# Kernel optimization log

Hardware: AMD Instinct MI355X
Metric: run time of the kernel (lower is better)

The kernel has to match this reference:

```python
import jax, jax.numpy as jnp
import numpy as np

NEG = -1e9  # effectively -inf for masked logits, grad-safe

def apply_rope(t, cos, sin):
    # t: [b, H, S, D]; cos/sin: [S, D] -> rotate-half RoPE
    d = t.shape[-1]
    t1, t2 = t[..., : d // 2], t[..., d // 2 :]
    rot = jnp.concatenate([-t2, t1], axis=-1)
    return t * cos[None, None] + rot * sin[None, None]


def setup_inputs() -> dict:
    key = jax.random.key(0)
    ks = jax.random.split(key, 8)
    b, S, d_in = 1, 4096, 2048
    H, G, D = 16, 4, 128
    d_out = H * D
    sc = 1.0 / np.sqrt(d_in)
    x = jax.random.normal(ks[0], (b, S, d_in), dtype=jnp.float32)
    # causal mask: True = masked (future positions)
    mask = jnp.triu(jnp.ones((S, S), dtype=bool), k=1)
    inv = 1.0 / (10000.0 ** (jnp.arange(0, D, 2, dtype=jnp.float32) / D))
    ang = jnp.arange(S, dtype=jnp.float32)[:, None] * inv[None, :]  # [S, D/2]
    ang = jnp.concatenate([ang, ang], axis=-1)                      # [S, D]
    cos, sin = jnp.cos(ang), jnp.sin(ang)
    Wq = jax.random.normal(ks[1], (d_out, d_in), dtype=jnp.float32) * sc
    Wk = jax.random.normal(ks[2], (G * D, d_in), dtype=jnp.float32) * sc
    Wv = jax.random.normal(ks[3], (G * D, d_in), dtype=jnp.float32) * sc
    Wo = jax.random.normal(ks[4], (d_in, d_out), dtype=jnp.float32) * sc
    return {"x": x, "mask": mask, "cos": cos, "sin": sin,
            "Wq": Wq, "Wk": Wk, "Wv": Wv, "Wo": Wo}


def reference(x, mask, cos, sin, Wq, Wk, Wv, Wo):
    b, S, d_in = x.shape
    G = Wk.shape[0] // cos.shape[-1]          # num_kv_groups
    D = cos.shape[-1]                          # head_dim
    H = Wq.shape[0] // D                       # num_heads
    n = H // G                                 # group_size
    q = (x @ Wq.T).reshape(b, S, H, D).transpose(0, 2, 1, 3)   # [b,H,S,D]
    k = (x @ Wk.T).reshape(b, S, G, D).transpose(0, 2, 1, 3)   # [b,G,S,D]
    v = (x @ Wv.T).reshape(b, S, G, D).transpose(0, 2, 1, 3)
    q = apply_rope(q, cos, sin)
    k = apply_rope(k, cos, sin)
    # GQA: group heads instead of repeat_interleave (head h -> group h // n)
    qg = q.reshape(b, G, n, S, D)
    scores = jnp.einsum('bgnqd,bgkd->bgnqk', qg, k)            # [b,G,n,S,S]
    scores = jnp.where(mask[None, None, None], NEG, scores)
    w = jax.nn.softmax(scores / np.sqrt(D), axis=-1)
    ctx = jnp.einsum('bgnqk,bgkd->bgnqd', w, v)                # [b,G,n,S,D]
    ctx = ctx.reshape(b, H, S, D).transpose(0, 2, 1, 3).reshape(b, S, H * D)
    return ctx @ Wo.T
```

## Files before the change

### kernel.cpp

```cpp
#include <hip/hip_runtime.h>

typedef __attribute__((ext_vector_type(8))) short bf16x8;
typedef __attribute__((ext_vector_type(4))) short bf16x4;
typedef __attribute__((ext_vector_type(8))) unsigned short u16x8;
typedef __attribute__((ext_vector_type(4))) float f32x4;

__device__ __forceinline__ unsigned short f2b(float f) {
  unsigned int u = __builtin_bit_cast(unsigned int, f);
  u += 0x7FFFu + ((u >> 16) & 1u);
  return (unsigned short)(u >> 16);
}
__device__ __forceinline__ float b2f(unsigned short h) {
  return __builtin_bit_cast(float, ((unsigned int)h) << 16);
}

__device__ __forceinline__ f32x4 mfma16x16x16(bf16x4 a, bf16x4 b, f32x4 c) {
#if __has_builtin(__builtin_amdgcn_mfma_f32_16x16x16bf16_1k)
  return __builtin_amdgcn_mfma_f32_16x16x16bf16_1k(a, b, c, 0, 0, 0);
#else
  asm volatile("v_mfma_f32_16x16x16_bf16 %0, %1, %2, %0" : "+v"(c) : "v"(a), "v"(b));
  return c;
#endif
}

#define AS1(p) (const __attribute__((address_space(1))) void*)(p)
#define AS3(p) (__attribute__((address_space(3))) void*)(p)

__device__ __forceinline__ void cvt8(const float* __restrict__ in,
                                     unsigned short* __restrict__ out,
                                     int i, float scale) {
  const float4* p = (const float4*)in + (size_t)i * 2;
  float4 a = p[0], b = p[1];
  u16x8 r;
  r[0] = f2b(a.x * scale); r[1] = f2b(a.y * scale);
  r[2] = f2b(a.z * scale); r[3] = f2b(a.w * scale);
  r[4] = f2b(b.x * scale); r[5] = f2b(b.y * scale);
  r[6] = f2b(b.z * scale); r[7] = f2b(b.w * scale);
  *((u16x8*)out + i) = r;
}

__global__ __launch_bounds__(256) void k_cvt_all(
    const float* __restrict__ x,  const float* __restrict__ Wq,
    const float* __restrict__ Wk, const float* __restrict__ Wv,
    const float* __restrict__ Wo, unsigned short* __restrict__ xb,
    unsigned short* __restrict__ wqkv, unsigned short* __restrict__ Wob,
    float sc) {
  int bid = blockIdx.x;
  int tid = threadIdx.x;
  if (bid < 4096)      cvt8(x,  xb,             (bid        ) * 256 + tid, 1.f);
  else if (bid < 6144) cvt8(Wq, wqkv,           (bid - 4096) * 256 + tid, sc);
  else if (bid < 6656) cvt8(Wk, wqkv + 4194304, (bid - 6144) * 256 + tid, 1.f);
  else if (bid < 7168) cvt8(Wv, wqkv + 5242880, (bid - 6656) * 256 + tid, 1.f);
  else                 cvt8(Wo, Wob,            (bid - 7168) * 256 + tid, 1.f);
}

__global__ __launch_bounds__(256) void k_post(unsigned short* __restrict__ qkv,
                                              const float* __restrict__ cosb,
                                              const float* __restrict__ sinb,
                                              unsigned short* __restrict__ vT) {
  __shared__ unsigned short tile[64][72];
  const int bid = blockIdx.x, t = threadIdx.x;
  if (bid < 2560) {
    int tid = bid * 256 + t;
    int oct = tid & 7;
    int hd  = (tid >> 3) % 20;
    int s   = (tid >> 3) / 20;
    unsigned short* p1 = qkv + (size_t)s * 3072 + hd * 128 + oct * 8;
    unsigned short* p2 = p1 + 64;
    u16x8 a = *(const u16x8*)p1;
    u16x8 b = *(const u16x8*)p2;
    const float4* cp = (const float4*)(cosb + (size_t)s * 128 + oct * 8);
    const float4* sp = (const float4*)(sinb + (size_t)s * 128 + oct * 8);
    float4 c0 = cp[0], c1 = cp[1], s0 = sp[0], s1 = sp[1];
    float cs[8] = {c0.x,c0.y,c0.z,c0.w,c1.x,c1.y,c1.z,c1.w};
    float sn[8] = {s0.x,s0.y,s0.z,s0.w,s1.x,s1.y,s1.z,s1.w};
    u16x8 ra, rb;
#pragma unroll
    for (int j = 0; j < 8; ++j) {
      float av = b2f(a[j]), bv = b2f(b[j]);
      ra[j] = f2b(av * cs[j] - bv * sn[j]);
      rb[j] = f2b(bv * cs[j] + av * sn[j]);
    }
    *(u16x8*)p1 = ra;
    *(u16x8*)p2 = rb;
  } else {
    int idx = bid - 2560;
    int bs = idx >> 3, bc = idx & 7;
#pragma unroll
    for (int i = 0; i < 2; ++i) {
      int c8 = t + 256 * i;
      int row = c8 >> 3, cb = c8 & 7;
      u16x8 v = *(const u16x8*)(qkv + (size_t)(bs * 64 + row) * 3072 + 2560 + bc * 64 + cb * 8);
#pragma unroll
      for (int j = 0; j < 8; ++j) tile[row][cb * 8 + j] = v[j];
    }
    __syncthreads();
#pragma unroll
    for (int i = 0; i < 2; ++i) {
      int c8 = t + 256 * i;
      int crow = c8 >> 3, sb = c8 & 7;
      u16x8 v;
#pragma unroll
      for (int j = 0; j < 8; ++j) v[j] = tile[sb * 8 + j][crow];
      *(u16x8*)(vT + (size_t)(bc * 64 + crow) * 4096 + bs * 64 + sb * 8) = v;
    }
  }
}

template <int OUTF32>
__global__ __launch_bounds__(256) void k_gemm_bt(
    const unsigned short* __restrict__ A, const unsigned short* __restrict__ B,
    void* __restrict__ C, int K, int lda, int ldb, int ldc) {
  __shared__ unsigned short As[128 * 64];
  __shared__ unsigned short Bs[128 * 64];
  const int t = threadIdx.x;
  const int lane = t & 63, w = t >> 6;
  const int wm = w >> 1, wn = w & 1;
  const int o = blockIdx.x + blockIdx.y * gridDim.x;
  const int xcd = o & 7, j = o >> 3;
  const int per = gridDim.x >> 3;
  const int bn = xcd * per + (j % per);
  const int bm = j / per;
  const unsigned short* Arow = A + (size_t)(bm * 128) * lda;
  const unsigned short* Brow = B + (size_t)(bn * 128) * ldb;

  f32x4 acc[4][4] = {};
  for (int kt = 0; kt < K; kt += 64) {
#pragma unroll
    for (int i = 0; i < 4; ++i) {
      int idx = i * 256 + t;
      int r = idx >> 3, blk = idx & 7;
      int sb = blk ^ (r & 7);
      __builtin_amdgcn_global_load_lds(AS1(Arow + (size_t)r * lda + kt + sb * 8),
                                       AS3(As + (i * 256 + w * 64) * 8), 16, 0, 0);
    }
#pragma unroll
    for (int i = 0; i < 4; ++i) {
      int idx = i * 256 + t;
      int r = idx >> 3, blk = idx & 7;
      int sb = blk ^ (r & 7);
      __builtin_amdgcn_global_load_lds(AS1(Brow + (size_t)r * ldb + kt + sb * 8),
                                       AS3(Bs + (i * 256 + w * 64) * 8), 16, 0, 0);
    }
    __syncthreads();
#pragma unroll
    for (int kk = 0; kk < 2; ++kk) {
      bf16x8 av[4], bv[4];
#pragma unroll
      for (int i = 0; i < 4; ++i) {
        int r = wm * 64 + i * 16 + (lane & 15);
        int off = (r * 128 + (kk * 32 + (lane >> 4) * 8) * 2) ^ ((r & 7) << 4);
        av[i] = *(const bf16x8*)((const char*)As + off);
      }
#pragma unroll
      for (int j2 = 0; j2 < 4; ++j2) {
        int r = wn * 64 + j2 * 16 + (lane & 15);
        int off = (r * 128 + (kk * 32 + (lane >> 4) * 8) * 2) ^ ((r & 7) << 4);
        bv[j2] = *(const bf16x8*)((const char*)Bs + off);
      }
#pragma unroll
      for (int i = 0; i < 4; ++i)
#pragma unroll
        for (int j2 = 0; j2 < 4; ++j2)
          acc[i][j2] = __builtin_amdgcn_mfma_f32_16x16x32_bf16(av[i], bv[j2], acc[i][j2], 0, 0, 0);
    }
    __syncthreads();
  }
#pragma unroll
  for (int i = 0; i < 4; ++i)
#pragma unroll
    for (int j2 = 0; j2 < 4; ++j2)
#pragma unroll
      for (int r = 0; r < 4; ++r) {
        int m = bm * 128 + wm * 64 + i * 16 + (lane >> 4) * 4 + r;
        int n = bn * 128 + wn * 64 + j2 * 16 + (lane & 15);
        float v = acc[i][j2][r];
        if (OUTF32) ((float*)C)[(size_t)m * ldc + n] = v;
        else        ((unsigned short*)C)[(size_t)m * ldc + n] = f2b(v);
      }
}

__device__ __forceinline__ void stage_k(const unsigned short* __restrict__ qk,
                                        unsigned short* __restrict__ dst,
                                        int kt, int g, int t, int w) {
#pragma unroll
  for (int i = 0; i < 4; ++i) {
    int idx = i * 256 + t;
    int r = idx >> 4, blk = idx & 15;
    int sb = (blk & 8) | ((blk ^ r) & 7);
    __builtin_amdgcn_global_load_lds(
        AS1(qk + (size_t)(kt * 64 + r) * 3072 + 2048 + g * 128 + sb * 8),
        AS3(dst + (i * 256 + w * 64) * 8), 16, 0, 0);
  }
}
__device__ __forceinline__ void stage_v(const unsigned short* __restrict__ vT,
                                        unsigned short* __restrict__ dst,
                                        int kt, int g, int t, int w) {
#pragma unroll
  for (int i = 0; i < 4; ++i) {
    int idx = i * 256 + t;
    int r = idx >> 3, blk = idx & 7;
    int sb = blk ^ (r & 7);
    __builtin_amdgcn_global_load_lds(
        AS1(vT + (size_t)(g * 128 + r) * 4096 + kt * 64 + sb * 8),
        AS3(dst + (i * 256 + w * 64) * 8), 16, 0, 0);
  }
}

__global__ __launch_bounds__(512, 1) void k_attn(const unsigned short* __restrict__ qk,
                                                 const unsigned short* __restrict__ vT,
                                                 unsigned short* __restrict__ ctx) {
  __shared__ unsigned short Ks[2][2][64 * 128];
  __shared__ unsigned short Vs[2][2][64 * 128];
  const int b = blockIdx.x >> 3;
  const int hp = blockIdx.x & 7;
  const int h0 = hp * 2, g = hp >> 1;
  const int t = threadIdx.x;
  const int grp = t >> 8;
  const int tg = t & 255;
  const int lane = t & 63, w4 = (t >> 6) & 3;
  const int l15 = lane & 15, lq = lane >> 4;

  float* ol = (float*)&Ks[0][0][0];
  float* ll = (float*)&Vs[0][0][0];

  for (int ph = 0; ph < 2; ++ph) {
    const int qt = ph ? 63 - b : b;
    const int ntot = qt + 1;
    const int m = (ntot + 1) >> 1;
    const int nB = ntot - m;
    const int kbase = grp ? m : 0;
    const int ntile = grp ? nB : m;
    const int qg = qt * 64 + w4 * 16 + l15;

    bf16x8 aq0[4], aq1[4];
    {
      const unsigned short* qb =
          qk + (size_t)(qt * 64 + w4 * 16 + l15) * 3072 + h0 * 128 + lq * 8;
#pragma unroll
      for (int sl = 0; sl < 4; ++sl) {
        aq0[sl] = *(const bf16x8*)(qb + sl * 32);
        aq1[sl] = *(const bf16x8*)(qb + 128 + sl * 32);
      }
    }
    f32x4 o0[8] = {}, o1[8] = {};
    float lsum0 = 0.f, lsum1 = 0.f;

    unsigned short* K0 = Ks[grp][0];
    unsigned short* K1 = Ks[grp][1];
    unsigned short* V0 = Vs[grp][0];
    unsigned short* V1 = Vs[grp][1];

    if (ntile > 0) {
      stage_k(qk, K0, kbase, g, tg, w4);
      stage_v(vT, V0, kbase, g, tg, w4);
    }
    asm volatile("s_waitcnt vmcnt(0)" ::: "memory");
    __builtin_amdgcn_s_barrier();

    auto tile = [&](const unsigned short* Kb, const unsigned short* Vb,
                    int kt, bool maskT) {
      f32x4 st0[4] = {}, st1[4] = {};
      __builtin_amdgcn_s_setprio(1);
#pragma unroll
      for (int sl = 0; sl < 4; ++sl)
#pragma unroll
        for (int nt = 0; nt < 4; ++nt) {
          int key = nt * 16 + l15;
          int off = (key * 256 + sl * 64 + lq * 16) ^ ((key & 7) << 4);
          bf16x8 bk = *(const bf16x8*)((const char*)Kb + off);
          st0[nt] = __builtin_amdgcn_mfma_f32_16x16x32_bf16(bk, aq0[sl], st0[nt], 0, 0, 0);
          st1[nt] = __builtin_amdgcn_mfma_f32_16x16x32_bf16(bk, aq1[sl], st1[nt], 0, 0, 0);
        }
      __builtin_amdgcn_s_setprio(0);

      bf16x4 pa0[4], pa1[4];
#pragma unroll
      for (int nt = 0; nt < 4; ++nt)
#pragma unroll
        for (int r = 0; r < 4; ++r) {
          float p0 = __builtin_amdgcn_exp2f(st0[nt][r]);
          float p1 = __builtin_amdgcn_exp2f(st1[nt][r]);
          if (maskT) {
            int key = kt * 64 + nt * 16 + lq * 4 + r;
            if (key > qg) { p0 = 0.f; p1 = 0.f; }
          }
          lsum0 += p0; lsum1 += p1;
          unsigned int u0 = __builtin_bit_cast(unsigned int, p0) + 0x8000u;
          unsigned int u1 = __builtin_bit_cast(unsigned int, p1) + 0x8000u;
          pa0[nt][r] = (short)(u0 >> 16);
          pa1[nt][r] = (short)(u1 >> 16);
        }

      __builtin_amdgcn_s_setprio(1);
#pragma unroll
      for (int nt = 0; nt < 4; ++nt)
#pragma unroll
        for (int dt = 0; dt < 8; ++dt) {
          int d = dt * 16 + l15;
          int off = (d * 128 + nt * 32 + lq * 8) ^ ((d & 7) << 4);
          bf16x4 vv = *(const bf16x4*)((const char*)Vb + off);
          o0[dt] = mfma16x16x16(pa0[nt], vv, o0[dt]);
          o1[dt] = mfma16x16x16(pa1[nt], vv, o1[dt]);
        }
      __builtin_amdgcn_s_setprio(0);
    };

    for (int i = 0; i < m; ++i) {
      const int cur = i & 1;
      if (i + 1 < ntile) {
        stage_k(qk, cur ? K0 : K1, kbase + i + 1, g, tg, w4);
        stage_v(vT, cur ? V0 : V1, kbase + i + 1, g, tg, w4);
      }
      if (i < ntile) {
        const int kt = kbase + i;
        tile(cur ? K1 : K0, cur ? V1 : V0, kt, kt == qt);
      }
      asm volatile("s_waitcnt vmcnt(0)" ::: "memory");
      __builtin_amdgcn_s_barrier();
    }

    float f0 = lsum0, f1 = lsum1;
    f0 += __shfl_xor(f0, 16); f0 += __shfl_xor(f0, 32);
    f1 += __shfl_xor(f1, 16); f1 += __shfl_xor(f1, 32);

    if (grp == 1) {
#pragma unroll
      for (int dt = 0; dt < 8; ++dt)
#pragma unroll
        for (int r = 0; r < 4; ++r) {
          ol[(dt * 4 + r) * 256 + tg]        = o0[dt][r];
          ol[(32 + dt * 4 + r) * 256 + tg]   = o1[dt][r];
        }
      if (lq == 0) {
        ll[w4 * 16 + l15]      = f0;
        ll[64 + w4 * 16 + l15] = f1;
      }
    }
    __builtin_amdgcn_s_barrier();
    if (grp == 0) {
#pragma unroll
      for (int dt = 0; dt < 8; ++dt)
#pragma unroll
        for (int r = 0; r < 4; ++r) {
          o0[dt][r] += ol[(dt * 4 + r) * 256 + tg];
          o1[dt][r] += ol[(32 + dt * 4 + r) * 256 + tg];
        }
      f0 += ll[w4 * 16 + l15];
      f1 += ll[64 + w4 * 16 + l15];
      float iq0[4], iq1[4];
#pragma unroll
      for (int r = 0; r < 4; ++r) {
        iq0[r] = 1.f / __shfl(f0, lq * 4 + r);
        iq1[r] = 1.f / __shfl(f1, lq * 4 + r);
      }
#pragma unroll
      for (int dt = 0; dt < 8; ++dt)
#pragma unroll
        for (int r = 0; r < 4; ++r) {
          int q = qt * 64 + w4 * 16 + lq * 4 + r;
          int c = h0 * 128 + dt * 16 + l15;
          ctx[(size_t)q * 2048 + c]       = f2b(o0[dt][r] * iq0[r]);
          ctx[(size_t)q * 2048 + c + 128] = f2b(o1[dt][r] * iq1[r]);
        }
    }
    __builtin_amdgcn_s_barrier();
  }
}

extern "C" void kernel_launch(void* const* d_in, const int* in_sizes, int n_in,
                              void* d_out, int out_size, void* d_ws, size_t ws_size,
                              hipStream_t stream) {
  const float* x    = (const float*)d_in[0];
  const float* cosb = (const float*)d_in[2];
  const float* sinb = (const float*)d_in[3];
  const float* Wq   = (const float*)d_in[4];
  const float* Wk   = (const float*)d_in[5];
  const float* Wv   = (const float*)d_in[6];
  const float* Wo   = (const float*)d_in[7];

  char* p = (char*)d_ws;
  unsigned short* xb   = (unsigned short*)p; p += (size_t)8388608 * 2;
  unsigned short* wqkv = (unsigned short*)p; p += (size_t)6291456 * 2;
  unsigned short* Wob  = (unsigned short*)p; p += (size_t)4194304 * 2;
  unsigned short* qkvb = (unsigned short*)p; p += (size_t)4096 * 3072 * 2;
  unsigned short* vTb  = (unsigned short*)p; p += (size_t)512 * 4096 * 2;
  unsigned short* ctx  = (unsigned short*)p; p += (size_t)4096 * 2048 * 2;
  if (ws_size < (size_t)(p - (char*)d_ws)) return;

  const float SC = 0.12751741f;

  k_cvt_all<<<9216, 256, 0, stream>>>(x, Wq, Wk, Wv, Wo, xb, wqkv, Wob, SC);

  k_gemm_bt<0><<<dim3(24, 32), 256, 0, stream>>>(xb, wqkv, qkvb, 2048, 2048, 2048, 3072);

  k_post<<<3072, 256, 0, stream>>>(qkvb, cosb, sinb, vTb);

  k_attn<<<256, 512, 0, stream>>>(qkvb, vTb, ctx);

  k_gemm_bt<1><<<dim3(16, 32), 256, 0, stream>>>(ctx, Wob, d_out, 2048, 2048, 2048, 2048);
}
```

Measured before the change: 233.8 us.

## Software-pipeline attention: compute next tile's QK/softmax before current PV

Restructures the key-tile loop so that the QK^T scores and exp for tile i+1 are computed before the PV accumulation of tile i, with K prefetched two tiles ahead and V one tile ahead. This lets the exp/convert VALU work of one tile sit alongside the MFMA work of the other, hiding softmax latency between matrix phases. It adds extra probability registers (current and next) and a prologue barrier, which raises register pressure and may lower occupancy.

```diff
diff --git a/kernel.cpp b/kernel.cpp
--- a/kernel.cpp
+++ b/kernel.cpp
@@ -245,21 +245,14 @@
     }
     f32x4 o0[8] = {}, o1[8] = {};
     float lsum0 = 0.f, lsum1 = 0.f;
+    bf16x4 paC0[4], paC1[4], paN0[4], paN1[4];
 
     unsigned short* K0 = Ks[grp][0];
     unsigned short* K1 = Ks[grp][1];
     unsigned short* V0 = Vs[grp][0];
     unsigned short* V1 = Vs[grp][1];
 
-    if (ntile > 0) {
-      stage_k(qk, K0, kbase, g, tg, w4);
-      stage_v(vT, V0, kbase, g, tg, w4);
-    }
-    asm volatile("s_waitcnt vmcnt(0)" ::: "memory");
-    __builtin_amdgcn_s_barrier();
-
-    auto tile = [&](const unsigned short* Kb, const unsigned short* Vb,
-                    int kt, bool maskT) {
+    auto qk_sm = [&](const unsigned short* Kb, int ktg, bf16x4* pA0, bf16x4* pA1) {
       f32x4 st0[4] = {}, st1[4] = {};
       __builtin_amdgcn_s_setprio(1);
 #pragma unroll
@@ -273,8 +266,7 @@
           st1[nt] = __builtin_amdgcn_mfma_f32_16x16x32_bf16(bk, aq1[sl], st1[nt], 0, 0, 0);
         }
       __builtin_amdgcn_s_setprio(0);
-
-      bf16x4 pa0[4], pa1[4];
+      const bool maskT = (ktg == qt);
 #pragma unroll
       for (int nt = 0; nt < 4; ++nt)
 #pragma unroll
@@ -282,16 +274,17 @@
           float p0 = __builtin_amdgcn_exp2f(st0[nt][r]);
           float p1 = __builtin_amdgcn_exp2f(st1[nt][r]);
           if (maskT) {
-            int key = kt * 64 + nt * 16 + lq * 4 + r;
+            int key = ktg * 64 + nt * 16 + lq * 4 + r;
             if (key > qg) { p0 = 0.f; p1 = 0.f; }
           }
           lsum0 += p0; lsum1 += p1;
           unsigned int u0 = __builtin_bit_cast(unsigned int, p0) + 0x8000u;
           unsigned int u1 = __builtin_bit_cast(unsigned int, p1) + 0x8000u;
-          pa0[nt][r] = (short)(u0 >> 16);
-          pa1[nt][r] = (short)(u1 >> 16);
-        }
-
+          pA0[nt][r] = (short)(u0 >> 16);
+          pA1[nt][r] = (short)(u1 >> 16);
+        }
+    };
+    auto pv = [&](const unsigned short* Vb, const bf16x4* pA0, const bf16x4* pA1) {
       __builtin_amdgcn_s_setprio(1);
 #pragma unroll
       for (int nt = 0; nt < 4; ++nt)
@@ -300,21 +293,35 @@
           int d = dt * 16 + l15;
           int off = (d * 128 + nt * 32 + lq * 8) ^ ((d & 7) << 4);
           bf16x4 vv = *(const bf16x4*)((const char*)Vb + off);
-          o0[dt] = mfma16x16x16(pa0[nt], vv, o0[dt]);
-          o1[dt] = mfma16x16x16(pa1[nt], vv, o1[dt]);
+          o0[dt] = mfma16x16x16(pA0[nt], vv, o0[dt]);
+          o1[dt] = mfma16x16x16(pA1[nt], vv, o1[dt]);
         }
       __builtin_amdgcn_s_setprio(0);
     };
 
+    if (ntile > 0) {
+      stage_k(qk, K0, kbase, g, tg, w4);
+      stage_v(vT, V0, kbase, g, tg, w4);
+    }
+    if (ntile > 1) stage_k(qk, K1, kbase + 1, g, tg, w4);
+    asm volatile("s_waitcnt vmcnt(0)" ::: "memory");
+    __builtin_amdgcn_s_barrier();
+    if (ntile > 0) qk_sm(K0, kbase, paC0, paC1);
+    __builtin_amdgcn_s_barrier();
+
     for (int i = 0; i < m; ++i) {
       const int cur = i & 1;
+      unsigned short* Kcur = cur ? K1 : K0;
+      unsigned short* Knxt = cur ? K0 : K1;
+      unsigned short* Vcur = cur ? V1 : V0;
+      unsigned short* Vnxt = cur ? V0 : V1;
+      if (i + 2 < ntile) stage_k(qk, Kcur, kbase + i + 2, g, tg, w4);
+      if (i + 1 < ntile) stage_v(vT, Vnxt, kbase + i + 1, g, tg, w4);
+      if (i + 1 < ntile) qk_sm(Knxt, kbase + i + 1, paN0, paN1);
+      if (i < ntile)     pv(Vcur, paC0, paC1);
       if (i + 1 < ntile) {
-        stage_k(qk, cur ? K0 : K1, kbase + i + 1, g, tg, w4);
-        stage_v(vT, cur ? V0 : V1, kbase + i + 1, g, tg, w4);
-      }
-      if (i < ntile) {
-        const int kt = kbase + i;
-        tile(cur ? K1 : K0, cur ? V1 : V0, kt, kt == qt);
+#pragma unroll
+        for (int nt = 0; nt < 4; ++nt) { paC0[nt] = paN0[nt]; paC1[nt] = paN1[nt]; }
       }
       asm volatile("s_waitcnt vmcnt(0)" ::: "memory");
       __builtin_amdgcn_s_barrier();
```

Result: slower. 240.6 us (+2.9%).

## Split K/V prefetch with partial vmcnt waits; drop XCD-aware GEMM block remap

Applied to the files above, without the earlier changes.

The attention loop now issues the next K tile load before the QK^T stage and the next V tile load after softmax. It uses counted vmcnt waits instead of full drains, so global loads for the following tile overlap with current compute. This adds an extra barrier per iteration and relies on exact per-thread load counts in stage_k and stage_v for correctness. Separately, the GEMM drops the XCD-aware block index swizzle and uses plain blockIdx mapping, which may change L2 locality across chiplets.

```diff
diff --git a/kernel.cpp b/kernel.cpp
--- a/kernel.cpp
+++ b/kernel.cpp
@@ -116,11 +116,7 @@
   const int t = threadIdx.x;
   const int lane = t & 63, w = t >> 6;
   const int wm = w >> 1, wn = w & 1;
-  const int o = blockIdx.x + blockIdx.y * gridDim.x;
-  const int xcd = o & 7, j = o >> 3;
-  const int per = gridDim.x >> 3;
-  const int bn = xcd * per + (j % per);
-  const int bm = j / per;
+  const int bn = blockIdx.x, bm = blockIdx.y;
   const unsigned short* Arow = A + (size_t)(bm * 128) * lda;
   const unsigned short* Brow = B + (size_t)(bn * 128) * ldb;
 
@@ -255,70 +251,77 @@
       stage_k(qk, K0, kbase, g, tg, w4);
       stage_v(vT, V0, kbase, g, tg, w4);
     }
-    asm volatile("s_waitcnt vmcnt(0)" ::: "memory");
-    __builtin_amdgcn_s_barrier();
-
-    auto tile = [&](const unsigned short* Kb, const unsigned short* Vb,
-                    int kt, bool maskT) {
-      f32x4 st0[4] = {}, st1[4] = {};
-      __builtin_amdgcn_s_setprio(1);
-#pragma unroll
-      for (int sl = 0; sl < 4; ++sl)
-#pragma unroll
-        for (int nt = 0; nt < 4; ++nt) {
-          int key = nt * 16 + l15;
-          int off = (key * 256 + sl * 64 + lq * 16) ^ ((key & 7) << 4);
-          bf16x8 bk = *(const bf16x8*)((const char*)Kb + off);
-          st0[nt] = __builtin_amdgcn_mfma_f32_16x16x32_bf16(bk, aq0[sl], st0[nt], 0, 0, 0);
-          st1[nt] = __builtin_amdgcn_mfma_f32_16x16x32_bf16(bk, aq1[sl], st1[nt], 0, 0, 0);
-        }
-      __builtin_amdgcn_s_setprio(0);
-
-      bf16x4 pa0[4], pa1[4];
-#pragma unroll
-      for (int nt = 0; nt < 4; ++nt)
-#pragma unroll
-        for (int r = 0; r < 4; ++r) {
-          float p0 = __builtin_amdgcn_exp2f(st0[nt][r]);
-          float p1 = __builtin_amdgcn_exp2f(st1[nt][r]);
-          if (maskT) {
-            int key = kt * 64 + nt * 16 + lq * 4 + r;
-            if (key > qg) { p0 = 0.f; p1 = 0.f; }
-          }
-          lsum0 += p0; lsum1 += p1;
-          unsigned int u0 = __builtin_bit_cast(unsigned int, p0) + 0x8000u;
-          unsigned int u1 = __builtin_bit_cast(unsigned int, p1) + 0x8000u;
-          pa0[nt][r] = (short)(u0 >> 16);
-          pa1[nt][r] = (short)(u1 >> 16);
-        }
-
-      __builtin_amdgcn_s_setprio(1);
-#pragma unroll
-      for (int nt = 0; nt < 4; ++nt)
-#pragma unroll
-        for (int dt = 0; dt < 8; ++dt) {
-          int d = dt * 16 + l15;
-          int off = (d * 128 + nt * 32 + lq * 8) ^ ((d & 7) << 4);
-          bf16x4 vv = *(const bf16x4*)((const char*)Vb + off);
-          o0[dt] = mfma16x16x16(pa0[nt], vv, o0[dt]);
-          o1[dt] = mfma16x16x16(pa1[nt], vv, o1[dt]);
-        }
-      __builtin_amdgcn_s_setprio(0);
-    };
 
     for (int i = 0; i < m; ++i) {
       const int cur = i & 1;
-      if (i + 1 < ntile) {
-        stage_k(qk, cur ? K0 : K1, kbase + i + 1, g, tg, w4);
-        stage_v(vT, cur ? V0 : V1, kbase + i + 1, g, tg, w4);
-      }
-      if (i < ntile) {
-        const int kt = kbase + i;
-        tile(cur ? K1 : K0, cur ? V1 : V0, kt, kt == qt);
-      }
-      asm volatile("s_waitcnt vmcnt(0)" ::: "memory");
+      const unsigned short* Kb = cur ? K1 : K0;
+      const unsigned short* Vb = cur ? V1 : V0;
+      const bool pre = (i + 1 < ntile);
+      const int kt = kbase + i;
+      const bool live = (i < ntile);
+      const bool maskT = live && (kt == qt);
+
+      if (pre) stage_k(qk, cur ? K0 : K1, kbase + i + 1, g, tg, w4);
+      if (pre) asm volatile("s_waitcnt vmcnt(8)" ::: "memory");
+      else     asm volatile("s_waitcnt vmcnt(4)" ::: "memory");
       __builtin_amdgcn_s_barrier();
-    }
+
+      f32x4 st0[4] = {}, st1[4] = {};
+      if (live) {
+        __builtin_amdgcn_s_setprio(1);
+#pragma unroll
+        for (int sl = 0; sl < 4; ++sl)
+#pragma unroll
+          for (int nt = 0; nt < 4; ++nt) {
+            int key = nt * 16 + l15;
+            int off = (key * 256 + sl * 64 + lq * 16) ^ ((key & 7) << 4);
+            bf16x8 bk = *(const bf16x8*)((const char*)Kb + off);
+            st0[nt] = __builtin_amdgcn_mfma_f32_16x16x32_bf16(bk, aq0[sl], st0[nt], 0, 0, 0);
+            st1[nt] = __builtin_amdgcn_mfma_f32_16x16x32_bf16(bk, aq1[sl], st1[nt], 0, 0, 0);
+          }
+        __builtin_amdgcn_s_setprio(0);
+      }
+      bf16x4 pa0[4], pa1[4];
+      if (live) {
+#pragma unroll
+        for (int nt = 0; nt < 4; ++nt)
+#pragma unroll
+          for (int r = 0; r < 4; ++r) {
+            float p0 = __builtin_amdgcn_exp2f(st0[nt][r]);
+            float p1 = __builtin_amdgcn_exp2f(st1[nt][r]);
+            if (maskT) {
+              int key = kt * 64 + nt * 16 + lq * 4 + r;
+              if (key > qg) { p0 = 0.f; p1 = 0.f; }
+            }
+            lsum0 += p0; lsum1 += p1;
+            unsigned int u0 = __builtin_bit_cast(unsigned int, p0) + 0x8000u;
+            unsigned int u1 = __builtin_bit_cast(unsigned int, p1) + 0x8000u;
+            pa0[nt][r] = (short)(u0 >> 16);
+            pa1[nt][r] = (short)(u1 >> 16);
+          }
+      }
+
+      if (pre) stage_v(vT, cur ? V0 : V1, kbase + i + 1, g, tg, w4);
+      if (pre) asm volatile("s_waitcnt vmcnt(8)" ::: "memory");
+      else     asm volatile("s_waitcnt vmcnt(0)" ::: "memory");
+      __builtin_amdgcn_s_barrier();
+
+      if (live) {
+        __builtin_amdgcn_s_setprio(1);
+#pragma unroll
+        for (int nt = 0; nt < 4; ++nt)
+#pragma unroll
+          for (int dt = 0; dt < 8; ++dt) {
+            int d = dt * 16 + l15;
+            int off = (d * 128 + nt * 32 + lq * 8) ^ ((d & 7) << 4);
+            bf16x4 vv = *(const bf16x4*)((const char*)Vb + off);
+            o0[dt] = mfma16x16x16(pa0[nt], vv, o0[dt]);
+            o1[dt] = mfma16x16x16(pa1[nt], vv, o1[dt]);
+          }
+        __builtin_amdgcn_s_setprio(0);
+      }
+    }
+    __builtin_amdgcn_s_barrier();
 
     float f0 = lsum0, f1 = lsum1;
     f0 += __shfl_xor(f0, 16); f0 += __shfl_xor(f0, 32);
```

Result: no change. 237.2 us (+1.4%).

## Use 256x256 double-buffered GEMM with split prefetch for QKV projection

Applied to the files above, without the earlier changes.

Adds a new 512-thread GEMM kernel with 256x256 output tiles, double-buffered LDS staging through direct global-to-LDS loads, and the next tile's prefetch split into two halves interleaved with the MFMA work. It uses the 16x16x32 bf16 MFMA and raises wave priority around the compute phases. The QKV projection now launches this kernel on a 12x16 grid, which gives more data reuse per block at the cost of only 192 blocks, about one wave on the device. The XCD-aware block remapping is also removed from the older GEMM, which is still used for the output projection.

```diff
diff --git a/kernel.cpp b/kernel.cpp
--- a/kernel.cpp
+++ b/kernel.cpp
@@ -107,6 +107,106 @@
   }
 }
 
+__global__ __launch_bounds__(512, 1) void k_gemm256(
+    const unsigned short* __restrict__ A, const unsigned short* __restrict__ B,
+    unsigned short* __restrict__ C, int K, int lda, int ldb, int ldc) {
+  __shared__ unsigned short As[2][256 * 64];
+  __shared__ unsigned short Bs[2][256 * 64];
+  const int t = threadIdx.x;
+  const int lane = t & 63, w = t >> 6;
+  const int wm = w >> 2, wn = w & 3;
+  const int l15 = lane & 15, lq = lane >> 4;
+  const int bn = blockIdx.x, bm = blockIdx.y;
+  const unsigned short* Arow = A + (size_t)(bm * 256) * lda;
+  const unsigned short* Brow = B + (size_t)(bn * 256) * ldb;
+  const int NT = K >> 6;
+
+  auto stage = [&](int buf, int kt, int q0, int q1) {
+#pragma unroll
+    for (int q = q0; q < q1; ++q) {
+      int idx = (q & 3) * 512 + t;
+      int r = idx >> 3, blk = idx & 7;
+      int sb = blk ^ (r & 7);
+      const unsigned short* src =
+          (q < 4 ? Arow + (size_t)r * lda : Brow + (size_t)r * ldb) + kt + sb * 8;
+      unsigned short* dst = (q < 4 ? As[buf] : Bs[buf]) + (size_t)idx * 8;
+      __builtin_amdgcn_global_load_lds(AS1(src), AS3(dst), 16, 0, 0);
+    }
+  };
+
+  f32x4 acc[8][4] = {};
+  stage(0, 0, 0, 8);
+
+  for (int tau = 0; tau < NT; ++tau) {
+    const int buf = tau & 1;
+    const char* Ab = (const char*)As[buf];
+    const char* Bb = (const char*)Bs[buf];
+    const bool pre = (tau + 1 < NT);
+    if (pre) stage(buf ^ 1, (tau + 1) << 6, 0, 4);
+    if (pre) asm volatile("s_waitcnt vmcnt(4)" ::: "memory");
+    else     asm volatile("s_waitcnt vmcnt(0)" ::: "memory");
+    __builtin_amdgcn_s_barrier();
+
+    bf16x8 bv[4][2];
+#pragma unroll
+    for (int j = 0; j < 4; ++j)
+#pragma unroll
+      for (int kk = 0; kk < 2; ++kk) {
+        int r = wn * 64 + j * 16 + l15;
+        int off = (r * 128 + (kk * 32 + lq * 8) * 2) ^ ((r & 7) << 4);
+        bv[j][kk] = *(const bf16x8*)(Bb + off);
+      }
+    __builtin_amdgcn_s_setprio(1);
+#pragma unroll
+    for (int i = 0; i < 4; ++i) {
+      bf16x8 av[2];
+#pragma unroll
+      for (int kk = 0; kk < 2; ++kk) {
+        int r = wm * 128 + i * 16 + l15;
+        int off = (r * 128 + (kk * 32 + lq * 8) * 2) ^ ((r & 7) << 4);
+        av[kk] = *(const bf16x8*)(Ab + off);
+      }
+#pragma unroll
+      for (int kk = 0; kk < 2; ++kk)
+#pragma unroll
+        for (int j = 0; j < 4; ++j)
+          acc[i][j] = __builtin_amdgcn_mfma_f32_16x16x32_bf16(av[kk], bv[j][kk], acc[i][j], 0, 0, 0);
+    }
+    __builtin_amdgcn_s_setprio(0);
+
+    if (pre) stage(buf ^ 1, (tau + 1) << 6, 4, 8);
+    __builtin_amdgcn_s_setprio(1);
+#pragma unroll
+    for (int i = 4; i < 8; ++i) {
+      bf16x8 av[2];
+#pragma unroll
+      for (int kk = 0; kk < 2; ++kk) {
+        int r = wm * 128 + i * 16 + l15;
+        int off = (r * 128 + (kk * 32 + lq * 8) * 2) ^ ((r & 7) << 4);
+        av[kk] = *(const bf16x8*)(Ab + off);
+      }
+#pragma unroll
+      for (int kk = 0; kk < 2; ++kk)
+#pragma unroll
+        for (int j = 0; j < 4; ++j)
+          acc[i][j] = __builtin_amdgcn_mfma_f32_16x16x32_bf16(av[kk], bv[j][kk], acc[i][j], 0, 0, 0);
+    }
+    __builtin_amdgcn_s_setprio(0);
+    __builtin_amdgcn_s_barrier();
+  }
+
+#pragma unroll
+  for (int i = 0; i < 8; ++i)
+#pragma unroll
+    for (int j = 0; j < 4; ++j)
+#pragma unroll
+      for (int r = 0; r < 4; ++r) {
+        int m = bm * 256 + wm * 128 + i * 16 + lq * 4 + r;
+        int n = bn * 256 + wn * 64 + j * 16 + l15;
+        C[(size_t)m * ldc + n] = f2b(acc[i][j][r]);
+      }
+}
+
 template <int OUTF32>
 __global__ __launch_bounds__(256) void k_gemm_bt(
     const unsigned short* __restrict__ A, const unsigned short* __restrict__ B,
@@ -116,11 +216,7 @@
   const int t = threadIdx.x;
   const int lane = t & 63, w = t >> 6;
   const int wm = w >> 1, wn = w & 1;
-  const int o = blockIdx.x + blockIdx.y * gridDim.x;
-  const int xcd = o & 7, j = o >> 3;
-  const int per = gridDim.x >> 3;
-  const int bn = xcd * per + (j % per);
-  const int bm = j / per;
+  const int bn = blockIdx.x, bm = blockIdx.y;
   const unsigned short* Arow = A + (size_t)(bm * 128) * lda;
   const unsigned short* Brow = B + (size_t)(bn * 128) * ldb;
 
@@ -392,7 +488,7 @@
 
   k_cvt_all<<<9216, 256, 0, stream>>>(x, Wq, Wk, Wv, Wo, xb, wqkv, Wob, SC);
 
-  k_gemm_bt<0><<<dim3(24, 32), 256, 0, stream>>>(xb, wqkv, qkvb, 2048, 2048, 2048, 3072);
+  k_gemm256<<<dim3(12, 16), 512, 0, stream>>>(xb, wqkv, qkvb, 2048, 2048, 2048, 3072);
 
   k_post<<<3072, 256, 0, stream>>>(qkvb, cosb, sinb, vTb);
 
```

New measurement: 232.6 us. Within noise of the previous version (-0.5%).
